# Kernel optimization log

Measured on AMD Instinct MI355X. Metric: run time of the kernel, lower is better.

The kernel has to match this reference:

```python
import jax, jax.numpy as jnp
import numpy as np

B, T, D, N = 16, 4096, 512, 3


def _window_sum(x, k):
    # x: [B, T, ...] -> sliding-window sum of size k, stride 1 -> [B, T-k+1, ...]
    c = jnp.cumsum(x, axis=1)
    c = jnp.concatenate([jnp.zeros_like(c[:, :1]), c], axis=1)
    return c[:, k:] - c[:, :-k]


def setup_inputs() -> dict:
    key = jax.random.key(0)
    ks = jax.random.split(key, 7)
    s_prev = jax.random.normal(ks[0], (B, D), jnp.float32)
    enc_hs = jax.random.normal(ks[1], (B, T, D), jnp.float32)
    # realistic padding mask: True = padded position
    lengths = jax.random.randint(ks[2], (B,), T // 2, T + 1)
    src_mask = jnp.arange(T)[None, :] >= lengths[:, None]
    scale = 1.0 / np.sqrt(D)
    Vw = jax.random.normal(ks[3], (N, D, D), jnp.float32) * scale
    Vb = jax.random.normal(ks[4], (N, D), jnp.float32) * 0.01
    Ww = jax.random.normal(ks[5], (N, D, D), jnp.float32) * scale
    Wb = jax.random.normal(ks[6], (N, D), jnp.float32) * 0.01
    return {"s_prev": s_prev, "enc_hs": enc_hs, "src_mask": src_mask,
            "Vw": Vw, "Vb": Vb, "Ww": Ww, "Wb": Wb}


def _level(s_prev, hs, mask, vw, vb, ww, wb):
    # hs: [B, L, D], mask: [B, L] (True = masked)
    # torch Linear: y = x @ W^T + b, weight is [out, in]
    v = jnp.einsum('bld,ed->ble', hs, vw) + vb            # V_i(hs)
    att = jnp.einsum('bd,bld->bl', s_prev, v)             # bmm(s_prev, V(hs)^T)
    att = jnp.where(mask, -jnp.inf, att)
    att = jax.nn.softmax(att, axis=-1)                    # [B, L]
    pooled = jnp.einsum('bl,bld->bd', att, hs)            # bmm(att, hs)
    ctx = pooled @ ww.T + wb                              # W_i(.)
    return ctx, att


def reference(s_prev, enc_hs, src_mask, Vw, Vb, Ww, Wb):
    ctx, att = _level(s_prev, enc_hs, src_mask, Vw[0], Vb[0], Ww[0], Wb[0])
    for i in range(1, N):
        k = i + 1
        hs_ngram = _window_sum(enc_hs, k) / k                      # AvgPool1d(k,1)
        n_mask = _window_sum(src_mask.astype(jnp.float32), k) > 0  # any masked in window
        c, _ = _level(s_prev, hs_ngram, n_mask, Vw[i], Vb[i], Ww[i], Wb[i])
        ctx = ctx + c
    return ctx, att
```

## Files before the change

### kernel.cpp

```cpp
#include <hip/hip_runtime.h>

#define BB 16
#define TT 4096
#define DD 512
#define NCHUNK 64

#define OFF_Q    64
#define OFF_P    (OFF_Q + 3*BB*DD)
#define OFF_W    (OFF_P + 3*BB*TT)
#define OFF_POOL (OFF_W + 3*BB*TT)
#define OFF_PART (OFF_POOL + 3*BB*DD)

__global__ void __launch_bounds__(1024) k_lengths(const unsigned char* mask, int* lengths) {
    __shared__ int sflag;
    const int tid = threadIdx.x;
    if (tid == 0) sflag = 0;
    __syncthreads();
    int f = 0;
    for (int idx = tid * 4 + 1; idx < BB * TT; idx += 1024 * 4)
        f |= (mask[idx] != 0);
    if (f) atomicOr(&sflag, 1);
    __syncthreads();
    const bool byte_layout = (sflag != 0);
    const int* m32 = (const int*)mask;
    const int b = tid >> 6;
    const int lane = tid & 63;
    int cnt = 0;
    if (byte_layout) {
        for (int t = lane; t < TT; t += 64) cnt += (mask[b * TT + t] != 0);
    } else {
        for (int t = lane; t < TT; t += 64) cnt += (m32[b * TT + t] != 0);
    }
    #pragma unroll
    for (int m = 32; m >= 1; m >>= 1) cnt += __shfl_xor(cnt, m, 64);
    if (lane == 0) lengths[b] = TT - cnt;
}

__global__ void __launch_bounds__(256) k_q(const float* __restrict__ s_prev,
                                           const float* __restrict__ Vw,
                                           float* __restrict__ q) {
    const int ib = blockIdx.x;
    const int b = ib % BB;
    const int i = ib / BB;
    const int d0 = threadIdx.x;
    const float* sp = s_prev + b * DD;
    const float* W = Vw + (size_t)i * DD * DD;
    float a0 = 0.f, a1 = 0.f;
    for (int e = 0; e < DD; e++) {
        const float se = sp[e];
        a0 += se * W[e * DD + d0];
        a1 += se * W[e * DD + d0 + 256];
    }
    q[(size_t)ib * DD + d0] = a0;
    q[(size_t)ib * DD + d0 + 256] = a1;
}

__global__ void __launch_bounds__(256) k_scores(const float* __restrict__ enc,
                                                const float* __restrict__ q,
                                                const int* __restrict__ lengths,
                                                float* __restrict__ p) {
    const int wid = blockIdx.x * 4 + (threadIdx.x >> 6);
    const int lane = threadIdx.x & 63;
    const int b = wid >> 12;
    const int t = wid & (TT - 1);
    if (t >= lengths[b]) return;
    const float4* e4 = (const float4*)(enc + (size_t)wid * DD);
    const float4 x0 = e4[lane * 2];
    const float4 x1 = e4[lane * 2 + 1];
    float acc[3];
    #pragma unroll
    for (int i = 0; i < 3; i++) {
        const float4* q4 = (const float4*)(q + (size_t)(i * BB + b) * DD);
        const float4 y0 = q4[lane * 2];
        const float4 y1 = q4[lane * 2 + 1];
        acc[i] = x0.x * y0.x + x0.y * y0.y + x0.z * y0.z + x0.w * y0.w
               + x1.x * y1.x + x1.y * y1.y + x1.z * y1.z + x1.w * y1.w;
    }
    #pragma unroll
    for (int m = 32; m >= 1; m >>= 1) {
        acc[0] += __shfl_xor(acc[0], m, 64);
        acc[1] += __shfl_xor(acc[1], m, 64);
        acc[2] += __shfl_xor(acc[2], m, 64);
    }
    if (lane == 0) {
        p[(size_t)(0 * BB + b) * TT + t] = acc[0];
        p[(size_t)(1 * BB + b) * TT + t] = acc[1];
        p[(size_t)(2 * BB + b) * TT + t] = acc[2];
    }
}

__global__ void __launch_bounds__(1024) k_softmax(const float* __restrict__ p,
                                                  const int* __restrict__ lengths,
                                                  float* __restrict__ w,
                                                  float* __restrict__ att_out) {
    __shared__ float sred[16];
    __shared__ float sbc;
    const int ib = blockIdx.x;
    const int b = ib % BB;
    const int i = ib / BB;
    const int k = i + 1;
    const float invk = 1.0f / (float)k;
    int V = lengths[b] - k + 1;
    if (V < 0) V = 0;
    const float* pp = p + (size_t)ib * TT;
    const int tid = threadIdx.x;

    float local = -3.4e38f;
    for (int l = tid; l < V; l += 1024) {
        float s = pp[l];
        if (k > 1) s += pp[l + 1];
        if (k > 2) s += pp[l + 2];
        local = fmaxf(local, s * invk);
    }
    float v = local;
    #pragma unroll
    for (int m = 32; m >= 1; m >>= 1) v = fmaxf(v, __shfl_xor(v, m, 64));
    if ((tid & 63) == 0) sred[tid >> 6] = v;
    __syncthreads();
    if (tid < 16) {
        float x = sred[tid];
        #pragma unroll
        for (int m = 8; m >= 1; m >>= 1) x = fmaxf(x, __shfl_xor(x, m, 16));
        if (tid == 0) sbc = x;
    }
    __syncthreads();
    const float mmax = sbc;
    __syncthreads();

    float lsum = 0.f;
    for (int l = tid; l < V; l += 1024) {
        float s = pp[l];
        if (k > 1) s += pp[l + 1];
        if (k > 2) s += pp[l + 2];
        lsum += __expf(s * invk - mmax);
    }
    v = lsum;
    #pragma unroll
    for (int m = 32; m >= 1; m >>= 1) v += __shfl_xor(v, m, 64);
    if ((tid & 63) == 0) sred[tid >> 6] = v;
    __syncthreads();
    if (tid < 16) {
        float x = sred[tid];
        #pragma unroll
        for (int m = 8; m >= 1; m >>= 1) x += __shfl_xor(x, m, 16);
        if (tid == 0) sbc = x;
    }
    __syncthreads();
    const float inv = 1.0f / sbc;

    for (int t = tid; t < TT; t += 1024) {
        float acc = 0.f;
        #pragma unroll
        for (int j = 0; j < 3; j++) {
            if (j < k) {
                const int l = t - j;
                if (l >= 0 && l < V) {
                    float s = pp[l];
                    if (k > 1) s += pp[l + 1];
                    if (k > 2) s += pp[l + 2];
                    acc += __expf(s * invk - mmax);
                }
            }
        }
        acc *= inv * invk;
        w[(size_t)ib * TT + t] = acc;
        if (i == 0) att_out[(size_t)b * TT + t] = acc;
    }
}

__global__ void __launch_bounds__(128) k_pool(const float* __restrict__ enc,
                                              const float* __restrict__ w,
                                              const int* __restrict__ lengths,
                                              float* __restrict__ part) {
    const int b = blockIdx.x;
    const int y = blockIdx.y;
    const int t0 = y * (TT / NCHUNK);
    const int d4 = threadIdx.x;
    int tend = t0 + (TT / NCHUNK);
    const int len = lengths[b];
    if (tend > len) tend = len;
    float4 a0 = {0, 0, 0, 0}, a1 = {0, 0, 0, 0}, a2 = {0, 0, 0, 0};
    const float* wb0 = w + (size_t)(0 * BB + b) * TT;
    const float* wb1 = w + (size_t)(1 * BB + b) * TT;
    const float* wb2 = w + (size_t)(2 * BB + b) * TT;
    for (int t = t0; t < tend; ++t) {
        const float4 x = ((const float4*)(enc + ((size_t)b * TT + t) * DD))[d4];
        const float w0 = wb0[t], w1 = wb1[t], w2 = wb2[t];
        a0.x += w0 * x.x; a0.y += w0 * x.y; a0.z += w0 * x.z; a0.w += w0 * x.w;
        a1.x += w1 * x.x; a1.y += w1 * x.y; a1.z += w1 * x.z; a1.w += w1 * x.w;
        a2.x += w2 * x.x; a2.y += w2 * x.y; a2.z += w2 * x.z; a2.w += w2 * x.w;
    }
    ((float4*)(part + ((size_t)((0 * NCHUNK + y) * BB) + b) * DD))[d4] = a0;
    ((float4*)(part + ((size_t)((1 * NCHUNK + y) * BB) + b) * DD))[d4] = a1;
    ((float4*)(part + ((size_t)((2 * NCHUNK + y) * BB) + b) * DD))[d4] = a2;
}

__global__ void __launch_bounds__(256) k_pool_reduce(const float* __restrict__ part,
                                                     float* __restrict__ pooled) {
    const int idx = blockIdx.x * 256 + threadIdx.x;
    const int i = idx / (BB * DD);
    const int bd = idx % (BB * DD);
    float s = 0.f;
    const float* base = part + (size_t)i * NCHUNK * BB * DD + bd;
    #pragma unroll 8
    for (int y = 0; y < NCHUNK; y++) s += base[(size_t)y * BB * DD];
    pooled[idx] = s;
}

__global__ void __launch_bounds__(256) k_ctx(const float* __restrict__ pooled,
                                             const float* __restrict__ Ww,
                                             const float* __restrict__ Wb,
                                             float* __restrict__ ctx) {
    const int wid = blockIdx.x * 4 + (threadIdx.x >> 6);
    const int lane = threadIdx.x & 63;
    const int b = wid >> 9;
    const int e = wid & 511;
    float acc = 0.f;
    #pragma unroll
    for (int i = 0; i < 3; i++) {
        const float4* pr = (const float4*)(pooled + (size_t)(i * BB + b) * DD);
        const float4* wr = (const float4*)(Ww + ((size_t)i * DD + e) * DD);
        const float4 p0 = pr[lane * 2], p1 = pr[lane * 2 + 1];
        const float4 w0 = wr[lane * 2], w1 = wr[lane * 2 + 1];
        acc += p0.x * w0.x + p0.y * w0.y + p0.z * w0.z + p0.w * w0.w
             + p1.x * w1.x + p1.y * w1.y + p1.z * w1.z + p1.w * w1.w;
    }
    #pragma unroll
    for (int m = 32; m >= 1; m >>= 1) acc += __shfl_xor(acc, m, 64);
    if (lane == 0)
        ctx[(size_t)b * DD + e] = acc + Wb[e] + Wb[DD + e] + Wb[2 * DD + e];
}

extern "C" void kernel_launch(void* const* d_in, const int* in_sizes, int n_in,
                              void* d_out, int out_size, void* d_ws, size_t ws_size,
                              hipStream_t stream) {
    const float* s_prev = (const float*)d_in[0];
    const float* enc    = (const float*)d_in[1];
    const void*  mask   = d_in[2];
    const float* Vw     = (const float*)d_in[3];
    const float* Ww     = (const float*)d_in[5];
    const float* Wb     = (const float*)d_in[6];

    float* out = (float*)d_out;
    float* ctx = out;
    float* att = out + BB * DD;

    float* W       = (float*)d_ws;
    int*   lengths = (int*)d_ws;
    float* q       = W + OFF_Q;
    float* p       = W + OFF_P;
    float* wbuf    = W + OFF_W;
    float* pooled  = W + OFF_POOL;
    float* part    = W + OFF_PART;

    k_lengths<<<1, 1024, 0, stream>>>((const unsigned char*)mask, lengths);
    k_q<<<3 * BB, 256, 0, stream>>>(s_prev, Vw, q);
    k_scores<<<BB * TT / 4, 256, 0, stream>>>(enc, q, lengths, p);
    k_softmax<<<3 * BB, 1024, 0, stream>>>(p, lengths, wbuf, att);
    k_pool<<<dim3(BB, NCHUNK), 128, 0, stream>>>(enc, wbuf, lengths, part);
    k_pool_reduce<<<3 * BB * DD / 256, 256, 0, stream>>>(part, pooled);
    k_ctx<<<BB * DD / 4, 256, 0, stream>>>(pooled, Ww, Wb, ctx);
}
```

Measured before the change: 278.4 us.

## Fuse scores, chunked online softmax and pooling into one pass over encoder states

Replaces the separate scores, softmax and pooling kernels with a fused kernel. Each block handles a 16-timestep chunk: it computes the three dot products, a local max and sum, and exp-weighted partial pooled vectors for all three n-gram levels. Combine and reduce kernels then rescale the per-chunk partials flash-softmax style, and the Vw projection is split into four column slices for more parallelism. This aims to read enc_hs once instead of twice and to drop the serial 48-block softmax, at the cost of a much larger partial buffer (256 chunks) that the reduce kernel must stream.

```diff
diff --git a/kernel.cpp b/kernel.cpp
--- a/kernel.cpp
+++ b/kernel.cpp
@@ -3,13 +3,20 @@
 #define BB 16
 #define TT 4096
 #define DD 512
-#define NCHUNK 64
-
-#define OFF_Q    64
-#define OFF_P    (OFF_Q + 3*BB*DD)
-#define OFF_W    (OFF_P + 3*BB*TT)
-#define OFF_POOL (OFF_W + 3*BB*TT)
-#define OFF_PART (OFF_POOL + 3*BB*DD)
+#define CH 16
+#define NY (TT/CH)
+#define NEG (-1.0e30f)
+
+#define OFF_Q     64
+#define OFF_QP    (OFF_Q + 3*BB*DD)
+#define OFF_P0    (OFF_QP + 4*3*BB*DD)
+#define OFF_M     (OFF_P0 + BB*TT)
+#define OFF_S     (OFF_M + 3*BB*NY)
+#define OFF_SC    (OFF_S + 3*BB*NY)
+#define OFF_MT    (OFF_SC + 3*BB*NY)
+#define OFF_TOT   (OFF_MT + 64)
+#define OFF_PART  (OFF_TOT + 64)
+#define OFF_POOL  (OFF_PART + 3*NY*BB*DD)
 
 __global__ void __launch_bounds__(1024) k_lengths(const unsigned char* mask, int* lengths) {
     __shared__ int sflag;
@@ -38,173 +45,214 @@
 
 __global__ void __launch_bounds__(256) k_q(const float* __restrict__ s_prev,
                                            const float* __restrict__ Vw,
-                                           float* __restrict__ q) {
-    const int ib = blockIdx.x;
+                                           float* __restrict__ qpart) {
+    const int blk = blockIdx.x;
+    const int ec = blk & 3;
+    const int ib = blk >> 2;
     const int b = ib % BB;
     const int i = ib / BB;
     const int d0 = threadIdx.x;
-    const float* sp = s_prev + b * DD;
-    const float* W = Vw + (size_t)i * DD * DD;
+    const float* sp = s_prev + b * DD + ec * 128;
+    const float* W = Vw + (size_t)i * DD * DD + (size_t)(ec * 128) * DD;
     float a0 = 0.f, a1 = 0.f;
-    for (int e = 0; e < DD; e++) {
+    for (int e = 0; e < 128; e++) {
         const float se = sp[e];
         a0 += se * W[e * DD + d0];
         a1 += se * W[e * DD + d0 + 256];
     }
-    q[(size_t)ib * DD + d0] = a0;
-    q[(size_t)ib * DD + d0 + 256] = a1;
-}
-
-__global__ void __launch_bounds__(256) k_scores(const float* __restrict__ enc,
-                                                const float* __restrict__ q,
-                                                const int* __restrict__ lengths,
-                                                float* __restrict__ p) {
-    const int wid = blockIdx.x * 4 + (threadIdx.x >> 6);
-    const int lane = threadIdx.x & 63;
-    const int b = wid >> 12;
-    const int t = wid & (TT - 1);
-    if (t >= lengths[b]) return;
-    const float4* e4 = (const float4*)(enc + (size_t)wid * DD);
-    const float4 x0 = e4[lane * 2];
-    const float4 x1 = e4[lane * 2 + 1];
-    float acc[3];
-    #pragma unroll
-    for (int i = 0; i < 3; i++) {
-        const float4* q4 = (const float4*)(q + (size_t)(i * BB + b) * DD);
-        const float4 y0 = q4[lane * 2];
-        const float4 y1 = q4[lane * 2 + 1];
-        acc[i] = x0.x * y0.x + x0.y * y0.y + x0.z * y0.z + x0.w * y0.w
-               + x1.x * y1.x + x1.y * y1.y + x1.z * y1.z + x1.w * y1.w;
-    }
-    #pragma unroll
-    for (int m = 32; m >= 1; m >>= 1) {
-        acc[0] += __shfl_xor(acc[0], m, 64);
-        acc[1] += __shfl_xor(acc[1], m, 64);
-        acc[2] += __shfl_xor(acc[2], m, 64);
-    }
-    if (lane == 0) {
-        p[(size_t)(0 * BB + b) * TT + t] = acc[0];
-        p[(size_t)(1 * BB + b) * TT + t] = acc[1];
-        p[(size_t)(2 * BB + b) * TT + t] = acc[2];
-    }
-}
-
-__global__ void __launch_bounds__(1024) k_softmax(const float* __restrict__ p,
-                                                  const int* __restrict__ lengths,
-                                                  float* __restrict__ w,
-                                                  float* __restrict__ att_out) {
-    __shared__ float sred[16];
-    __shared__ float sbc;
-    const int ib = blockIdx.x;
-    const int b = ib % BB;
-    const int i = ib / BB;
-    const int k = i + 1;
-    const float invk = 1.0f / (float)k;
-    int V = lengths[b] - k + 1;
-    if (V < 0) V = 0;
-    const float* pp = p + (size_t)ib * TT;
+    qpart[(size_t)blk * DD + d0] = a0;
+    qpart[(size_t)blk * DD + d0 + 256] = a1;
+}
+
+__global__ void __launch_bounds__(256) k_q_reduce(const float* __restrict__ qpart,
+                                                  float* __restrict__ q) {
+    const int idx = blockIdx.x * 256 + threadIdx.x;
+    const int ib = idx / DD;
+    const int d = idx % DD;
+    float s = 0.f;
+    #pragma unroll
+    for (int ec = 0; ec < 4; ec++) s += qpart[(size_t)(ib * 4 + ec) * DD + d];
+    q[idx] = s;
+}
+
+__global__ void __launch_bounds__(256) k_fused(const float* __restrict__ enc,
+                                               const float* __restrict__ q,
+                                               const int* __restrict__ lengths,
+                                               float* __restrict__ p0,
+                                               float* __restrict__ mbuf,
+                                               float* __restrict__ sbuf,
+                                               float* __restrict__ part) {
+    __shared__ float sp[CH + 2][3];
+    __shared__ float svs[3][CH];
+    __shared__ float su[3][CH];
+    __shared__ float sm[3];
+    const int b = blockIdx.x;
+    const int y = blockIdx.y;
+    const int t0 = y * CH;
+    const int len = lengths[b];
     const int tid = threadIdx.x;
-
-    float local = -3.4e38f;
-    for (int l = tid; l < V; l += 1024) {
-        float s = pp[l];
-        if (k > 1) s += pp[l + 1];
-        if (k > 2) s += pp[l + 2];
-        local = fmaxf(local, s * invk);
-    }
-    float v = local;
-    #pragma unroll
-    for (int m = 32; m >= 1; m >>= 1) v = fmaxf(v, __shfl_xor(v, m, 64));
-    if ((tid & 63) == 0) sred[tid >> 6] = v;
-    __syncthreads();
-    if (tid < 16) {
-        float x = sred[tid];
-        #pragma unroll
-        for (int m = 8; m >= 1; m >>= 1) x = fmaxf(x, __shfl_xor(x, m, 16));
-        if (tid == 0) sbc = x;
-    }
-    __syncthreads();
-    const float mmax = sbc;
-    __syncthreads();
-
-    float lsum = 0.f;
-    for (int l = tid; l < V; l += 1024) {
-        float s = pp[l];
-        if (k > 1) s += pp[l + 1];
-        if (k > 2) s += pp[l + 2];
-        lsum += __expf(s * invk - mmax);
-    }
-    v = lsum;
-    #pragma unroll
-    for (int m = 32; m >= 1; m >>= 1) v += __shfl_xor(v, m, 64);
-    if ((tid & 63) == 0) sred[tid >> 6] = v;
-    __syncthreads();
-    if (tid < 16) {
-        float x = sred[tid];
-        #pragma unroll
-        for (int m = 8; m >= 1; m >>= 1) x += __shfl_xor(x, m, 16);
-        if (tid == 0) sbc = x;
-    }
-    __syncthreads();
-    const float inv = 1.0f / sbc;
-
-    for (int t = tid; t < TT; t += 1024) {
-        float acc = 0.f;
-        #pragma unroll
-        for (int j = 0; j < 3; j++) {
-            if (j < k) {
-                const int l = t - j;
-                if (l >= 0 && l < V) {
-                    float s = pp[l];
-                    if (k > 1) s += pp[l + 1];
-                    if (k > 2) s += pp[l + 2];
-                    acc += __expf(s * invk - mmax);
-                }
+    if (t0 >= len) {
+        if (tid < 3) {
+            mbuf[(size_t)(tid * BB + b) * NY + y] = NEG;
+            sbuf[(size_t)(tid * BB + b) * NY + y] = 0.f;
+        }
+        return;
+    }
+    const int wv = tid >> 6, lane = tid & 63;
+
+    const float4* q40 = (const float4*)(q + (size_t)(0 * BB + b) * DD);
+    const float4* q41 = (const float4*)(q + (size_t)(1 * BB + b) * DD);
+    const float4* q42 = (const float4*)(q + (size_t)(2 * BB + b) * DD);
+    const float4 qa0 = q40[lane], qb0 = q40[64 + lane];
+    const float4 qa1 = q41[lane], qb1 = q41[64 + lane];
+    const float4 qa2 = q42[lane], qb2 = q42[64 + lane];
+    #pragma unroll
+    for (int rr = 0; rr < 5; rr++) {
+        if (rr == 4 && wv >= 2) break;
+        const int r = (rr < 4) ? (wv + rr * 4) : (CH + wv);
+        const int t = t0 + r;
+        float d0 = 0.f, d1 = 0.f, d2 = 0.f;
+        if (t < len) {
+            const float4* e4 = (const float4*)(enc + ((size_t)b * TT + t) * DD);
+            const float4 x0 = e4[lane], x1 = e4[64 + lane];
+            d0 = x0.x*qa0.x + x0.y*qa0.y + x0.z*qa0.z + x0.w*qa0.w
+               + x1.x*qb0.x + x1.y*qb0.y + x1.z*qb0.z + x1.w*qb0.w;
+            d1 = x0.x*qa1.x + x0.y*qa1.y + x0.z*qa1.z + x0.w*qa1.w
+               + x1.x*qb1.x + x1.y*qb1.y + x1.z*qb1.z + x1.w*qb1.w;
+            d2 = x0.x*qa2.x + x0.y*qa2.y + x0.z*qa2.z + x0.w*qa2.w
+               + x1.x*qb2.x + x1.y*qb2.y + x1.z*qb2.z + x1.w*qb2.w;
+            #pragma unroll
+            for (int m = 32; m >= 1; m >>= 1) {
+                d0 += __shfl_xor(d0, m, 64);
+                d1 += __shfl_xor(d1, m, 64);
+                d2 += __shfl_xor(d2, m, 64);
             }
         }
-        acc *= inv * invk;
-        w[(size_t)ib * TT + t] = acc;
-        if (i == 0) att_out[(size_t)b * TT + t] = acc;
-    }
-}
-
-__global__ void __launch_bounds__(128) k_pool(const float* __restrict__ enc,
-                                              const float* __restrict__ w,
-                                              const int* __restrict__ lengths,
-                                              float* __restrict__ part) {
-    const int b = blockIdx.x;
-    const int y = blockIdx.y;
-    const int t0 = y * (TT / NCHUNK);
-    const int d4 = threadIdx.x;
-    int tend = t0 + (TT / NCHUNK);
-    const int len = lengths[b];
-    if (tend > len) tend = len;
-    float4 a0 = {0, 0, 0, 0}, a1 = {0, 0, 0, 0}, a2 = {0, 0, 0, 0};
-    const float* wb0 = w + (size_t)(0 * BB + b) * TT;
-    const float* wb1 = w + (size_t)(1 * BB + b) * TT;
-    const float* wb2 = w + (size_t)(2 * BB + b) * TT;
-    for (int t = t0; t < tend; ++t) {
-        const float4 x = ((const float4*)(enc + ((size_t)b * TT + t) * DD))[d4];
-        const float w0 = wb0[t], w1 = wb1[t], w2 = wb2[t];
-        a0.x += w0 * x.x; a0.y += w0 * x.y; a0.z += w0 * x.z; a0.w += w0 * x.w;
-        a1.x += w1 * x.x; a1.y += w1 * x.y; a1.z += w1 * x.z; a1.w += w1 * x.w;
-        a2.x += w2 * x.x; a2.y += w2 * x.y; a2.z += w2 * x.z; a2.w += w2 * x.w;
-    }
-    ((float4*)(part + ((size_t)((0 * NCHUNK + y) * BB) + b) * DD))[d4] = a0;
-    ((float4*)(part + ((size_t)((1 * NCHUNK + y) * BB) + b) * DD))[d4] = a1;
-    ((float4*)(part + ((size_t)((2 * NCHUNK + y) * BB) + b) * DD))[d4] = a2;
-}
-
-__global__ void __launch_bounds__(256) k_pool_reduce(const float* __restrict__ part,
-                                                     float* __restrict__ pooled) {
+        if (lane == 0) {
+            sp[r][0] = d0; sp[r][1] = d1; sp[r][2] = d2;
+            if (rr < 4 && t < len) p0[(size_t)b * TT + t] = d0;
+        }
+    }
+    __syncthreads();
+
+    if (tid < 48) {
+        const int i = tid / CH, r = tid % CH;
+        const int l = t0 + r;
+        const bool valid = l < (len - i);
+        float s = sp[r][i];
+        if (i > 0) s += sp[r + 1][i];
+        if (i > 1) s += sp[r + 2][i];
+        svs[i][r] = valid ? s * (1.0f / (float)(i + 1)) : NEG;
+    }
+    __syncthreads();
+    if (tid < 3) {
+        float m = NEG;
+        #pragma unroll
+        for (int r = 0; r < CH; r++) m = fmaxf(m, svs[tid][r]);
+        sm[tid] = m;
+    }
+    __syncthreads();
+    if (tid < 48) {
+        const int i = tid / CH, r = tid % CH;
+        const bool valid = (t0 + r) < (len - i);
+        su[i][r] = valid ? __expf(svs[i][r] - sm[i]) : 0.f;
+    }
+    __syncthreads();
+    if (tid < 3) {
+        float s = 0.f;
+        #pragma unroll
+        for (int r = 0; r < CH; r++) s += su[tid][r];
+        mbuf[(size_t)(tid * BB + b) * NY + y] = sm[tid];
+        sbuf[(size_t)(tid * BB + b) * NY + y] = s;
+    }
+    __syncthreads();
+
+    const int d = tid * 2;
+    const float* col = enc + (size_t)b * TT * DD + d;
+    float2 va, vb2, vc;
+    {
+        const int t = t0;
+        va  = (t     < TT) ? *(const float2*)(col + (size_t)t * DD)       : make_float2(0.f, 0.f);
+        vb2 = (t + 1 < TT) ? *(const float2*)(col + (size_t)(t + 1) * DD) : make_float2(0.f, 0.f);
+    }
+    float2 a0 = {0, 0}, a1 = {0, 0}, a2 = {0, 0};
+    #pragma unroll
+    for (int r = 0; r < CH; r++) {
+        const int t = t0 + r;
+        vc = (t + 2 < TT) ? *(const float2*)(col + (size_t)(t + 2) * DD) : make_float2(0.f, 0.f);
+        const float u0 = su[0][r], u1 = su[1][r], u2 = su[2][r];
+        const float w1x = va.x + vb2.x, w1y = va.y + vb2.y;
+        const float w2x = w1x + vc.x,   w2y = w1y + vc.y;
+        a0.x += u0 * va.x;  a0.y += u0 * va.y;
+        a1.x += u1 * w1x;   a1.y += u1 * w1y;
+        a2.x += u2 * w2x;   a2.y += u2 * w2y;
+        va = vb2; vb2 = vc;
+    }
+    a1.x *= 0.5f; a1.y *= 0.5f;
+    a2.x *= (1.0f / 3.0f); a2.y *= (1.0f / 3.0f);
+    float* pt = part + (size_t)y * BB * DD + (size_t)b * DD + d;
+    *(float2*)(pt)                        = a0;
+    *(float2*)(pt + (size_t)NY * BB * DD)     = a1;
+    *(float2*)(pt + (size_t)2 * NY * BB * DD) = a2;
+}
+
+__global__ void __launch_bounds__(256) k_combine(const float* __restrict__ mbuf,
+                                                 const float* __restrict__ sbuf,
+                                                 float* __restrict__ scale,
+                                                 float* __restrict__ mtot,
+                                                 float* __restrict__ tot) {
+    const int g = blockIdx.x * 4 + (threadIdx.x >> 6);
+    const int lane = threadIdx.x & 63;
+    const float* mv = mbuf + (size_t)g * NY;
+    const float* sv = sbuf + (size_t)g * NY;
+    float ml[4], sl[4];
+    float m = NEG;
+    #pragma unroll
+    for (int j = 0; j < 4; j++) {
+        ml[j] = mv[lane * 4 + j];
+        sl[j] = sv[lane * 4 + j];
+        m = fmaxf(m, ml[j]);
+    }
+    #pragma unroll
+    for (int s = 32; s >= 1; s >>= 1) m = fmaxf(m, __shfl_xor(m, s, 64));
+    float t = 0.f;
+    #pragma unroll
+    for (int j = 0; j < 4; j++) t += sl[j] * __expf(ml[j] - m);
+    #pragma unroll
+    for (int s = 32; s >= 1; s >>= 1) t += __shfl_xor(t, s, 64);
+    const float inv = 1.0f / t;
+    #pragma unroll
+    for (int j = 0; j < 4; j++)
+        scale[(size_t)g * NY + lane * 4 + j] = __expf(ml[j] - m) * inv;
+    if (lane == 0) { mtot[g] = m; tot[g] = t; }
+}
+
+__global__ void __launch_bounds__(256) k_reduce(const float* __restrict__ part,
+                                                const float* __restrict__ scale,
+                                                float* __restrict__ pooled) {
     const int idx = blockIdx.x * 256 + threadIdx.x;
-    const int i = idx / (BB * DD);
-    const int bd = idx % (BB * DD);
+    const int ib = idx / DD;
+    const int d = idx % DD;
+    const int i = ib / BB, b = ib % BB;
+    const float* sc = scale + (size_t)ib * NY;
+    const float* base = part + (size_t)i * NY * BB * DD + (size_t)b * DD + d;
     float s = 0.f;
-    const float* base = part + (size_t)i * NCHUNK * BB * DD + bd;
     #pragma unroll 8
-    for (int y = 0; y < NCHUNK; y++) s += base[(size_t)y * BB * DD];
+    for (int y = 0; y < NY; y++) s += base[(size_t)y * BB * DD] * sc[y];
     pooled[idx] = s;
+}
+
+__global__ void __launch_bounds__(256) k_att(const float* __restrict__ p0,
+                                             const int* __restrict__ lengths,
+                                             const float* __restrict__ mtot,
+                                             const float* __restrict__ tot,
+                                             float* __restrict__ att) {
+    const int idx = blockIdx.x * 256 + threadIdx.x;
+    const int b = idx >> 12;
+    const int t = idx & (TT - 1);
+    const float m = mtot[b];
+    const float inv = 1.0f / tot[b];
+    att[idx] = (t < lengths[b]) ? __expf(p0[idx] - m) * inv : 0.f;
 }
 
 __global__ void __launch_bounds__(256) k_ctx(const float* __restrict__ pooled,
@@ -220,8 +268,8 @@
     for (int i = 0; i < 3; i++) {
         const float4* pr = (const float4*)(pooled + (size_t)(i * BB + b) * DD);
         const float4* wr = (const float4*)(Ww + ((size_t)i * DD + e) * DD);
-        const float4 p0 = pr[lane * 2], p1 = pr[lane * 2 + 1];
-        const float4 w0 = wr[lane * 2], w1 = wr[lane * 2 + 1];
+        const float4 p0 = pr[lane], p1 = pr[64 + lane];
+        const float4 w0 = wr[lane], w1 = wr[64 + lane];
         acc += p0.x * w0.x + p0.y * w0.y + p0.z * w0.z + p0.w * w0.w
              + p1.x * w1.x + p1.y * w1.y + p1.z * w1.z + p1.w * w1.w;
     }
@@ -248,16 +296,22 @@
     float* W       = (float*)d_ws;
     int*   lengths = (int*)d_ws;
     float* q       = W + OFF_Q;
-    float* p       = W + OFF_P;
-    float* wbuf    = W + OFF_W;
+    float* qpart   = W + OFF_QP;
+    float* p0      = W + OFF_P0;
+    float* mbuf    = W + OFF_M;
+    float* sbuf    = W + OFF_S;
+    float* scale   = W + OFF_SC;
+    float* mtot    = W + OFF_MT;
+    float* tot     = W + OFF_TOT;
+    float* part    = W + OFF_PART;
     float* pooled  = W + OFF_POOL;
-    float* part    = W + OFF_PART;
 
     k_lengths<<<1, 1024, 0, stream>>>((const unsigned char*)mask, lengths);
-    k_q<<<3 * BB, 256, 0, stream>>>(s_prev, Vw, q);
-    k_scores<<<BB * TT / 4, 256, 0, stream>>>(enc, q, lengths, p);
-    k_softmax<<<3 * BB, 1024, 0, stream>>>(p, lengths, wbuf, att);
-    k_pool<<<dim3(BB, NCHUNK), 128, 0, stream>>>(enc, wbuf, lengths, part);
-    k_pool_reduce<<<3 * BB * DD / 256, 256, 0, stream>>>(part, pooled);
+    k_q<<<192, 256, 0, stream>>>(s_prev, Vw, qpart);
+    k_q_reduce<<<3 * BB * DD / 256, 256, 0, stream>>>(qpart, q);
+    k_fused<<<dim3(BB, NY), 256, 0, stream>>>(enc, q, lengths, p0, mbuf, sbuf, part);
+    k_combine<<<12, 256, 0, stream>>>(mbuf, sbuf, scale, mtot, tot);
+    k_reduce<<<3 * BB * DD / 256, 256, 0, stream>>>(part, scale, pooled);
+    k_att<<<BB * TT / 256, 256, 0, stream>>>(p0, lengths, mtot, tot, att);
     k_ctx<<<BB * DD / 4, 256, 0, stream>>>(pooled, Ww, Wb, ctx);
 }
```

Result: faster. 266.6 us (-4.2%).
